# Optimization experiments

Hardware: AMD Instinct MI355X
Metric: run time of the kernel (lower is better)

## Reference

```python
import jax, jax.numpy as jnp
import numpy as np

N_HEADS = 16

def _rotate_half(t):
    # t: [B, H, T, hs]; split last dim in half, return cat(-x2, x1)
    hs = t.shape[-1]
    x1, x2 = t[..., : hs // 2], t[..., hs // 2 :]
    return jnp.concatenate((-x2, x1), axis=-1)

def _rope_pos(T, hs, dtype):
    inv_freq = 1.0 / (10000.0 ** (jnp.arange(0, hs, 2, dtype=jnp.float32) / hs))
    freqs = jnp.arange(T, dtype=jnp.float32)[:, None] * inv_freq[None, :]  # [T, hs/2]
    pos = jnp.concatenate((freqs, freqs), axis=-1)  # [T, hs]
    return pos

def setup_inputs() -> dict:
    key = jax.random.key(0)
    ks = jax.random.split(key, 5)
    d = 2048
    x = jax.random.normal(ks[0], (2, 2048, d), dtype=jnp.float32)
    W_attn = jax.random.normal(ks[1], (d, 3 * d), dtype=jnp.float32) * (1.0 / np.sqrt(d))
    b_attn = jax.random.normal(ks[2], (3 * d,), dtype=jnp.float32) * 0.02
    W_proj = jax.random.normal(ks[3], (d, d), dtype=jnp.float32) * (1.0 / np.sqrt(d))
    b_proj = jax.random.normal(ks[4], (d,), dtype=jnp.float32) * 0.02
    return {"x": x, "W_attn": W_attn, "b_attn": b_attn, "W_proj": W_proj, "b_proj": b_proj}

def reference(x, W_attn, b_attn, W_proj, b_proj):
    B, T, C = x.shape
    nh = N_HEADS
    hs = C // nh
    qkv = x @ W_attn + b_attn  # [B, T, 3C]
    q, k, v = jnp.split(qkv, 3, axis=-1)
    # [B, T, C] -> [B, nh, T, hs]
    def to_heads(t):
        return t.reshape(B, T, nh, hs).transpose(0, 2, 1, 3)
    q, k, v = to_heads(q), to_heads(k), to_heads(v)
    # RoPE
    pos = _rope_pos(T, hs, x.dtype)  # [T, hs]
    cos, sin = jnp.cos(pos).astype(x.dtype), jnp.sin(pos).astype(x.dtype)
    q = q * cos + _rotate_half(q) * sin
    k = k * cos + _rotate_half(k) * sin
    # causal SDPA
    scale = 1.0 / np.sqrt(hs)
    scores = jnp.einsum('bhqd,bhkd->bhqk', q, k) * scale  # [B, nh, T, T]
    causal = jnp.tril(jnp.ones((T, T), dtype=bool))
    scores = jnp.where(causal, scores, jnp.finfo(scores.dtype).min)
    att = jax.nn.softmax(scores, axis=-1)
    out = jnp.einsum('bhqk,bhkd->bhqd', att, v)  # [B, nh, T, hs]
    y = out.transpose(0, 2, 1, 3).reshape(B, T, C)
    return y @ W_proj + b_proj
```

## Files before the change

kernel.cpp:

```cpp
#include <hip/hip_runtime.h>
#include <stdint.h>

typedef unsigned short u16;
typedef __attribute__((ext_vector_type(8))) short short8;
typedef __attribute__((ext_vector_type(4))) float f32x4;
typedef __attribute__((ext_vector_type(4))) unsigned short u16x4;

#define DEV __device__ __forceinline__

DEV u16 f2bf(float f) {
  union { float f; unsigned u; } v; v.f = f;
  unsigned r = v.u + 0x7fffu + ((v.u >> 16) & 1u);
  return (u16)(r >> 16);
}
DEV float bf2f(u16 b) {
  union { unsigned u; float f; } v; v.u = ((unsigned)b) << 16;
  return v.f;
}
DEV void gload_lds16(const void* g, void* l) {
  __builtin_amdgcn_global_load_lds((const __attribute__((address_space(1))) void*)g,
                                   (__attribute__((address_space(3))) void*)l,
                                   16, 0, 0);
}
DEV void block_barrier() {
  asm volatile("" ::: "memory");
  __builtin_amdgcn_s_barrier();
  asm volatile("" ::: "memory");
}

__global__ void k_conv(const float* __restrict__ in, u16* __restrict__ out, int n4) {
  int i = blockIdx.x * blockDim.x + threadIdx.x;
  if (i >= n4) return;
  const f32x4 v = *(const f32x4*)(in + (size_t)i * 4);
  u16x4 o;
  o[0] = f2bf(v[0]); o[1] = f2bf(v[1]); o[2] = f2bf(v[2]); o[3] = f2bf(v[3]);
  *(u16x4*)(out + (size_t)i * 4) = o;
}

__global__ void k_tconv(const float* __restrict__ in, u16* __restrict__ out, int R, int C) {
  __shared__ float tile[32][33];
  int c0 = blockIdx.x * 32, r0 = blockIdx.y * 32;
  int tx = threadIdx.x, ty = threadIdx.y;
#pragma unroll
  for (int j = 0; j < 32; j += 8)
    tile[ty + j][tx] = in[(size_t)(r0 + ty + j) * C + (c0 + tx)];
  __syncthreads();
#pragma unroll
  for (int j = 0; j < 32; j += 8)
    out[(size_t)(c0 + ty + j) * R + (r0 + tx)] = f2bf(tile[tx][ty + j]);
}

__global__ __launch_bounds__(512, 2) void k_gemmqkv(const u16* __restrict__ A,
                                                    const u16* __restrict__ Bt,
                                                    const float* __restrict__ bias,
                                                    u16* __restrict__ qh,
                                                    u16* __restrict__ kh,
                                                    u16* __restrict__ vt) {
  const int Kld = 2048, nt = 32;
  __shared__ __align__(16) short smem[4][256 * 64];
  const int tid = threadIdx.x;
  const int wid = tid >> 6, lane = tid & 63;
  const int gx = gridDim.x;
  const int nwg = gx * gridDim.y;
  const int orig = blockIdx.y * gx + blockIdx.x;
  const int lg = (orig & 7) * (nwg >> 3) + (orig >> 3);
  const int bm = (lg % gx) * 256, bn = (lg / gx) * 256;
  const int wr = wid >> 2, wc = wid & 3;
  const int r = lane & 15, kq = lane >> 4, r7 = lane & 7;

  int aoff[4], boff[4], lbase[4];
#pragma unroll
  for (int j = 0; j < 4; ++j) {
    int c = j * 512 + wid * 64 + lane;
    int row = c >> 3, ch = c & 7;
    aoff[j] = (bm + row) * Kld + (ch ^ (row & 7)) * 8;
    boff[j] = (bn + row) * Kld + (ch ^ (row & 7)) * 8;
    lbase[j] = (j * 512 + wid * 64) * 16;
  }

#define STG_A(k0, buf, j) gload_lds16(A + aoff[j] + (k0), (char*)&smem[(buf)][0] + lbase[j])
#define STG_B(k0, buf, j) gload_lds16(Bt + boff[j] + (k0), (char*)&smem[2 + (buf)][0] + lbase[j])
#define RD_A(AF, MH, KK)                                                        \
  _Pragma("unroll")                                                             \
  for (int m2 = 0; m2 < 4; ++m2)                                                \
    AF[m2] = *(const short8*)&As[(wr * 128 + (MH) * 64 + m2 * 16 + r) * 64      \
                                 + (((KK) * 4 + kq) ^ r7) * 8];
#define RD_B(KK)                                                                \
  _Pragma("unroll")                                                             \
  for (int nf = 0; nf < 4; ++nf)                                                \
    bfr[KK][nf] = *(const short8*)&Bs[(wc * 64 + nf * 16 + r) * 64              \
                                      + (((KK) * 4 + kq) ^ r7) * 8];
#define PH_MFMA(AF, MH, KK)                                                     \
  __builtin_amdgcn_s_setprio(1);                                                \
  _Pragma("unroll")                                                             \
  for (int m2 = 0; m2 < 4; ++m2)                                                \
    _Pragma("unroll")                                                           \
    for (int nf = 0; nf < 4; ++nf)                                              \
      acc[(MH) * 4 + m2][nf] = __builtin_amdgcn_mfma_f32_16x16x32_bf16(         \
          AF[m2], bfr[KK][nf], acc[(MH) * 4 + m2][nf], 0, 0, 0);                \
  __builtin_amdgcn_s_setprio(0);

  f32x4 acc[8][4];
  const f32x4 zero = {0.f, 0.f, 0.f, 0.f};
#pragma unroll
  for (int i = 0; i < 8; ++i)
#pragma unroll
    for (int j = 0; j < 4; ++j) acc[i][j] = zero;

#pragma unroll
  for (int j = 0; j < 4; ++j) STG_A(0, 0, j);
#pragma unroll
  for (int j = 0; j < 4; ++j) STG_B(0, 0, j);
#pragma unroll
  for (int j = 0; j < 4; ++j) STG_B(64, 1, j);
  asm volatile("s_waitcnt vmcnt(4)" ::: "memory");
  block_barrier();

#pragma unroll 1
  for (int t = 0; t < nt; ++t) {
    const int cur = t & 1, nxt = cur ^ 1;
    const short* As = &smem[cur][0];
    const short* Bs = &smem[2 + cur][0];
    const int kA = (t + 1) * 64, kB = (t + 2) * 64;
    const bool sA = (t + 1 < nt), sB = (t + 2 < nt);
    short8 bfr[2][4];
    short8 af[4];

    RD_B(0)
    RD_A(af, 0, 0)
    if (sA) { STG_A(kA, nxt, 0); STG_A(kA, nxt, 1); }
    block_barrier();
    PH_MFMA(af, 0, 0)
    block_barrier();

    RD_B(1)
    RD_A(af, 0, 1)
    if (sA) { STG_A(kA, nxt, 2); STG_A(kA, nxt, 3); }
    block_barrier();
    PH_MFMA(af, 0, 1)
    block_barrier();

    RD_A(af, 1, 0)
    if (sB) { STG_B(kB, cur, 0); STG_B(kB, cur, 1); }
    block_barrier();
    PH_MFMA(af, 1, 0)
    block_barrier();

    RD_A(af, 1, 1)
    if (sB) { STG_B(kB, cur, 2); STG_B(kB, cur, 3); }
    block_barrier();
    PH_MFMA(af, 1, 1)
    if (t + 1 < nt) {
      if (sB) asm volatile("s_waitcnt vmcnt(4)" ::: "memory");
      else    asm volatile("s_waitcnt vmcnt(0)" ::: "memory");
    }
    block_barrier();
  }
#undef STG_A
#undef STG_B
#undef RD_A
#undef RD_B
#undef PH_MFMA

  const int by = lg / gx;
  const int part = by >> 3;
  const int b_ = bm >> 11;
  const int tb = bm & 2047;
  const int hbase = (bn & 2047) >> 7;
  u16* ob = (u16*)&smem[0][0];

#pragma unroll
  for (int nf = 0; nf < 4; ++nf) {
    int nl = wc * 64 + nf * 16 + r;
    float bv = bias[bn + nl];
#pragma unroll
    for (int mf = 0; mf < 8; ++mf) {
      int mlb = wr * 128 + mf * 16 + kq * 4;
#pragma unroll
      for (int i = 0; i < 4; ++i) {
        int ml = mlb + i;
        int cl = (part == 2)
          ? (nl ^ (((ml >> 2) & 3) << 4) ^ (((ml >> 4) & 7) << 1))
          : (nl ^ (((ml >> 2) & 3) << 4));
        ob[ml * 256 + cl] = f2bf(acc[mf][nf][i] + bv);
      }
    }
  }
  block_barrier();

  if (part == 2) {
#pragma unroll 1
    for (int iter = 0; iter < 32; ++iter) {
      int dl = iter * 8 + wid;
      int hh = hbase + (dl >> 7), d = dl & 127;
      int tl4 = lane * 4;
      int cl = dl ^ ((lane & 3) << 4) ^ (((lane >> 2) & 7) << 1);
      u16x4 o;
#pragma unroll
      for (int j = 0; j < 4; ++j) o[j] = ob[(tl4 + j) * 256 + cl];
      *(u16x4*)(vt + ((size_t)(b_ * 16 + hh) * 128 + d) * 2048 + tb + tl4) = o;
    }
  } else {
    u16* dst = part ? kh : qh;
    const float qscale = part ? 1.0f : 0.12751744766834352f;
    const int nl2 = lane * 4;
    const int hh = hbase + (nl2 >> 7);
    const int d0 = nl2 & 127;
    const int hi = (nl2 >> 6) & 1;
    float inv0 = exp2f((float)(nl2 & 63) * -0.20762050593045077f);
    const float k1 = 0.8659643233600653f;
    float invj[4];
    invj[0] = inv0; invj[1] = inv0 * k1; invj[2] = invj[1] * k1; invj[3] = invj[2] * k1;
#pragma unroll 1
    for (int iter = 0; iter < 32; ++iter) {
      int tl = iter * 8 + wid;
      float tg = (float)(tb + tl);
      int xr = ((tl >> 2) & 3) << 4;
      int base = tl * 256 + (nl2 ^ xr);
      int pbase = tl * 256 + ((nl2 ^ 64) ^ xr);
      u16x4 o;
#pragma unroll
      for (int j = 0; j < 4; ++j) {
        float vo = bf2f(ob[base + j]);
        float vp = bf2f(ob[pbase + j]);
        float sn, cs;
        sincosf(tg * invj[j], &sn, &cs);
        float vr = hi ? (vo * cs + vp * sn) : (vo * cs - vp * sn);
        o[j] = f2bf(vr * qscale);
      }
      *(u16x4*)(dst + ((size_t)(b_ * 16 + hh) * 2048 + (tb + tl)) * 128 + d0) = o;
    }
  }
}

template <bool OUT_BF16, bool SPLITK>
__global__ __launch_bounds__(512, 2) void k_gemm3(const u16* __restrict__ A,
                                                  const u16* __restrict__ Bt,
                                                  const float* __restrict__ bias,
                                                  void* __restrict__ Cv,
                                                  int M, int N, int Kld, int nkt) {
  __shared__ __align__(16) short lA[2][256 * 64];
  __shared__ __align__(16) short lB[2][256 * 64];
  const int tid = threadIdx.x;
  const int wid = tid >> 6, lane = tid & 63;
  const int gx = gridDim.x;
  const int nwg = gx * gridDim.y;
  const int orig = blockIdx.y * gx + blockIdx.x;
  const int lg = (orig & 7) * (nwg >> 3) + (orig >> 3);
  const int bm = (lg % gx) * 256, bn = (lg / gx) * 256;
  const int wr = wid >> 2, wc = wid & 3;
  const int r = lane & 15, kq = lane >> 4, r7 = lane & 7;
  const int kz = SPLITK ? blockIdx.z * (nkt << 6) : 0;

  int aoff[4], boff[4], lbase[4];
#pragma unroll
  for (int j = 0; j < 4; ++j) {
    int c = j * 512 + wid * 64 + lane;
    int row = c >> 3, ch = c & 7;
    aoff[j] = (bm + row) * Kld + kz + (ch ^ (row & 7)) * 8;
    boff[j] = (bn + row) * Kld + kz + (ch ^ (row & 7)) * 8;
    lbase[j] = (j * 512 + wid * 64) * 16;
  }

#define STG_A(k0, buf, j) gload_lds16(A + aoff[j] + (k0), (char*)&lA[(buf)][0] + lbase[j])
#define STG_B(k0, buf, j) gload_lds16(Bt + boff[j] + (k0), (char*)&lB[(buf)][0] + lbase[j])
#define RD_A(AF, MH, KK)                                                        \
  _Pragma("unroll")                                                             \
  for (int m2 = 0; m2 < 4; ++m2)                                                \
    AF[m2] = *(const short8*)&As[(wr * 128 + (MH) * 64 + m2 * 16 + r) * 64      \
                                 + (((KK) * 4 + kq) ^ r7) * 8];
#define RD_B(KK)                                                                \
  _Pragma("unroll")                                                             \
  for (int nf = 0; nf < 4; ++nf)                                                \
    bfr[KK][nf] = *(const short8*)&Bs[(wc * 64 + nf * 16 + r) * 64              \
                                      + (((KK) * 4 + kq) ^ r7) * 8];
#define PH_MFMA(AF, MH, KK)                                                     \
  __builtin_amdgcn_s_setprio(1);                                                \
  _Pragma("unroll")                                                             \
  for (int m2 = 0; m2 < 4; ++m2)                                                \
    _Pragma("unroll")                                                           \
    for (int nf = 0; nf < 4; ++nf)                                              \
      acc[(MH) * 4 + m2][nf] = __builtin_amdgcn_mfma_f32_16x16x32_bf16(         \
          AF[m2], bfr[KK][nf], acc[(MH) * 4 + m2][nf], 0, 0, 0);                \
  __builtin_amdgcn_s_setprio(0);

  f32x4 acc[8][4];
  const f32x4 zero = {0.f, 0.f, 0.f, 0.f};
#pragma unroll
  for (int i = 0; i < 8; ++i)
#pragma unroll
    for (int j = 0; j < 4; ++j) acc[i][j] = zero;

  const int nt = nkt;

#pragma unroll
  for (int j = 0; j < 4; ++j) STG_A(0, 0, j);
#pragma unroll
  for (int j = 0; j < 4; ++j) STG_B(0, 0, j);
  if (nt > 1) {
#pragma unroll
    for (int j = 0; j < 4; ++j) STG_B(64, 1, j);
    asm volatile("s_waitcnt vmcnt(4)" ::: "memory");
  } else {
    asm volatile("s_waitcnt vmcnt(0)" ::: "memory");
  }
  block_barrier();

#pragma unroll 1
  for (int t = 0; t < nt; ++t) {
    const int cur = t & 1, nxt = cur ^ 1;
    const short* As = &lA[cur][0];
    const short* Bs = &lB[cur][0];
    const int kA = (t + 1) * 64, kB = (t + 2) * 64;
    const bool sA = (t + 1 < nt), sB = (t + 2 < nt);
    short8 bfr[2][4];
    short8 af[4];

    RD_B(0)
    RD_A(af, 0, 0)
    if (sA) { STG_A(kA, nxt, 0); STG_A(kA, nxt, 1); }
    block_barrier();
    PH_MFMA(af, 0, 0)
    block_barrier();

    RD_B(1)
    RD_A(af, 0, 1)
    if (sA) { STG_A(kA, nxt, 2); STG_A(kA, nxt, 3); }
    block_barrier();
    PH_MFMA(af, 0, 1)
    block_barrier();

    RD_A(af, 1, 0)
    if (sB) { STG_B(kB, cur, 0); STG_B(kB, cur, 1); }
    block_barrier();
    PH_MFMA(af, 1, 0)
    block_barrier();

    RD_A(af, 1, 1)
    if (sB) { STG_B(kB, cur, 2); STG_B(kB, cur, 3); }
    block_barrier();
    PH_MFMA(af, 1, 1)
    if (t + 1 < nt) {
      if (sB) asm volatile("s_waitcnt vmcnt(4)" ::: "memory");
      else    asm volatile("s_waitcnt vmcnt(0)" ::: "memory");
    }
    block_barrier();
  }
#undef STG_A
#undef STG_B
#undef RD_A
#undef RD_B
#undef PH_MFMA

#pragma unroll
  for (int mf = 0; mf < 8; ++mf)
#pragma unroll
    for (int nf = 0; nf < 4; ++nf) {
      int n = bn + wc * 64 + nf * 16 + r;
      float bv = SPLITK ? 0.f : bias[n];
#pragma unroll
      for (int i = 0; i < 4; ++i) {
        int m = bm + wr * 128 + mf * 16 + kq * 4 + i;
        float val = acc[mf][nf][i] + bv;
        if (SPLITK)
          ((float*)Cv)[(size_t)blockIdx.z * M * N + (size_t)m * N + n] = val;
        else if (OUT_BF16)
          ((u16*)Cv)[(size_t)m * N + n] = f2bf(val);
        else
          ((float*)Cv)[(size_t)m * N + n] = val;
      }
    }
}

__global__ void k_fadd(const float* __restrict__ p, const float* __restrict__ bias,
                       float* __restrict__ y, int n4) {
  const int half4 = 2097152;
  for (int i = blockIdx.x * blockDim.x + threadIdx.x; i < n4; i += gridDim.x * blockDim.x) {
    f32x4 a = *(const f32x4*)(p + (size_t)i * 4);
    f32x4 b = *(const f32x4*)(p + (size_t)(i + half4) * 4);
    f32x4 bv = *(const f32x4*)(bias + ((i & 511) << 2));
    f32x4 o = a + b + bv;
    *(f32x4*)(y + (size_t)i * 4) = o;
  }
}

__global__ __launch_bounds__(256) void k_attn(const u16* __restrict__ qh,
                                              const u16* __restrict__ kh,
                                              const u16* __restrict__ vt,
                                              u16* __restrict__ out) {
  __shared__ __align__(16) short lK[2][64 * 128];
  __shared__ __align__(16) short lV[2][128 * 64];
  __shared__ __align__(16) short lP[64 * 64];
  const int tid = threadIdx.x, wid = tid >> 6, lane = tid & 63;
  const int p = blockIdx.x, h = blockIdx.y, b = blockIdx.z;
  const size_t bh = (size_t)b * 16 + h;
  const u16* qb = qh + bh * 2048 * 128;
  const u16* kb = kh + bh * 2048 * 128;
  const u16* vb = vt + bh * 128 * 2048;
  const int r = lane & 15, kq = lane >> 4;
  const int r7 = r & 7;
  const int wrow = wid * 16;

  int koff[4], voff[4];
#pragma unroll
  for (int i = 0; i < 4; ++i) {
    int ci = (wid * 4 + i) * 64 + lane;
    int krow = ci >> 4, kch = ci & 15;
    koff[i] = krow * 128 + ((kch ^ (krow & 7)) * 8);
    int vrow = ci >> 3, vch = ci & 7;
    voff[i] = vrow * 2048 + ((vch ^ (vrow & 7)) * 8);
  }

#pragma unroll 1
  for (int seg = 0; seg < 2; ++seg) {
    const int j = seg ? 31 - p : p;
    const int q0 = j * 64;
    const int nkt = j + 1;

    short8 qa[4];
#pragma unroll
    for (int kk = 0; kk < 4; ++kk)
      qa[kk] = *(const short8*)(qb + (size_t)(q0 + wrow + r) * 128 + kk * 32 + kq * 8);

    f32x4 O[8];
    const f32x4 zero = {0.f, 0.f, 0.f, 0.f};
#pragma unroll
    for (int nf = 0; nf < 8; ++nf) O[nf] = zero;
    float lp[4] = {0.f, 0.f, 0.f, 0.f};

#pragma unroll
    for (int i = 0; i < 4; ++i) {
      gload_lds16(kb + koff[i], (char*)&lK[0][0] + (wid * 4 + i) * 1024);
      gload_lds16(vb + voff[i], (char*)&lV[0][0] + (wid * 4 + i) * 1024);
    }

#pragma unroll 1
    for (int kt = 0; kt < nkt; ++kt) {
      const int cur = kt & 1;
      if (kt + 1 < nkt) {
        const size_t kbase = (size_t)(kt + 1) * 8192, vbase = (size_t)(kt + 1) * 64;
#pragma unroll
        for (int i = 0; i < 4; ++i) {
          gload_lds16(kb + kbase + koff[i], (char*)&lK[cur ^ 1][0] + (wid * 4 + i) * 1024);
          gload_lds16(vb + vbase + voff[i], (char*)&lV[cur ^ 1][0] + (wid * 4 + i) * 1024);
        }
        asm volatile("s_waitcnt vmcnt(8)" ::: "memory");
      } else {
        asm volatile("s_waitcnt vmcnt(0)" ::: "memory");
      }
      block_barrier();

      f32x4 S[4];
#pragma unroll
      for (int nf = 0; nf < 4; ++nf) S[nf] = zero;
#pragma unroll
      for (int kk = 0; kk < 4; ++kk) {
        short8 kf[4];
#pragma unroll
        for (int nf = 0; nf < 4; ++nf)
          kf[nf] = *(const short8*)&lK[cur][(nf * 16 + r) * 128 + ((kk * 4 + kq) ^ r7) * 8];
#pragma unroll
        for (int nf = 0; nf < 4; ++nf)
          S[nf] = __builtin_amdgcn_mfma_f32_16x16x32_bf16(qa[kk], kf[nf], S[nf], 0, 0, 0);
      }

      const bool diag = (kt == nkt - 1);
#pragma unroll
      for (int nf = 0; nf < 4; ++nf)
#pragma unroll
        for (int i = 0; i < 4; ++i) {
          float pv = exp2f(S[nf][i]);
          if (diag) {
            int kg = kt * 64 + nf * 16 + r;
            int qg = q0 + wrow + kq * 4 + i;
            pv = (kg > qg) ? 0.f : pv;
          }
          lp[i] += pv;
          int row = wrow + kq * 4 + i;
          int cl = (nf * 2 + (r >> 3)) ^ ((kq * 4 + i) & 7);
          lP[row * 64 + cl * 8 + r7] = (short)f2bf(pv);
        }

#pragma unroll
      for (int kk = 0; kk < 2; ++kk) {
        short8 pa = *(const short8*)&lP[(wrow + r) * 64 + ((kk * 4 + kq) ^ r7) * 8];
#pragma unroll
        for (int nf = 0; nf < 8; ++nf) {
          short8 vf = *(const short8*)&lV[cur][(nf * 16 + r) * 64 + ((kk * 4 + kq) ^ r7) * 8];
          O[nf] = __builtin_amdgcn_mfma_f32_16x16x32_bf16(pa, vf, O[nf], 0, 0, 0);
        }
      }
      asm volatile("s_waitcnt lgkmcnt(0)" ::: "memory");
      block_barrier();
    }

    float inv[4];
#pragma unroll
    for (int i = 0; i < 4; ++i) {
      float v = lp[i];
      v += __shfl_xor(v, 1);
      v += __shfl_xor(v, 2);
      v += __shfl_xor(v, 4);
      v += __shfl_xor(v, 8);
      inv[i] = 1.f / v;
    }
#pragma unroll
    for (int nf = 0; nf < 8; ++nf)
#pragma unroll
      for (int i = 0; i < 4; ++i) {
        int qg = q0 + wrow + kq * 4 + i;
        out[(size_t)(b * 2048 + qg) * 2048 + h * 128 + nf * 16 + r] = f2bf(O[nf][i] * inv[i]);
      }
  }
}

extern "C" void kernel_launch(void* const* d_in, const int* in_sizes, int n_in,
                              void* d_out, int out_size, void* d_ws, size_t ws_size,
                              hipStream_t stream) {
  const float* x      = (const float*)d_in[0];
  const float* W_attn = (const float*)d_in[1];
  const float* b_attn = (const float*)d_in[2];
  const float* W_proj = (const float*)d_in[3];
  const float* b_proj = (const float*)d_in[4];
  float* y = (float*)d_out;

  u16* xb     = (u16*)d_ws;
  u16* wqkvT  = xb     + (size_t)4096 * 2048;
  u16* wprojT = wqkvT  + (size_t)6144 * 2048;
  u16* qkv    = wprojT + (size_t)2048 * 2048;
  u16* qh     = qkv    + (size_t)4096 * 6144;
  u16* kh     = qh     + (size_t)4096 * 2048;
  u16* vt     = kh     + (size_t)4096 * 2048;
  u16* attout = vt     + (size_t)4096 * 2048;
  if (ws_size < (size_t)83886080 * 2) return;

  float* pproj = (float*)qkv;

  k_conv<<<8192, 256, 0, stream>>>(x, xb, 2097152);
  k_tconv<<<dim3(192, 64), dim3(32, 8), 0, stream>>>(W_attn, wqkvT, 2048, 6144);
  k_tconv<<<dim3(64, 64), dim3(32, 8), 0, stream>>>(W_proj, wprojT, 2048, 2048);
  k_gemmqkv<<<dim3(16, 24), 512, 0, stream>>>(xb, wqkvT, b_attn, qh, kh, vt);
  k_attn<<<dim3(16, 16, 2), 256, 0, stream>>>(qh, kh, vt, attout);
  k_gemm3<false, true><<<dim3(16, 8, 2), 512, 0, stream>>>(attout, wprojT, b_proj, pproj, 4096, 2048, 2048, 16);
  k_fadd<<<2048, 256, 0, stream>>>(pproj, b_proj, y, 2097152);
}
```

Measured before the change: 319.8 us.

## Precompute RoPE sin/cos table and widen attention blocks to 128 query rows

Adds a small kernel that precomputes cos/sin tables for RoPE so the QKV GEMM epilogue loads them instead of calling sincosf per element. The attention kernel now uses 512 threads (8 waves) covering 128 query rows per block, halving the grid and sharing each K/V tile load across twice as many query rows. The diagonal masking now spans two key tiles. This trades more LDS and a larger block for less redundant K/V traffic and less transcendental work, and it reduces the number of blocks available for load balancing.

```diff
diff --git a/kernel.cpp b/kernel.cpp
--- a/kernel.cpp
+++ b/kernel.cpp
@@ -50,12 +50,22 @@
     out[(size_t)(c0 + ty + j) * R + (r0 + tx)] = f2bf(tile[tx][ty + j]);
 }
 
+__global__ void k_rtab(float* __restrict__ ct, float* __restrict__ st) {
+  int id = blockIdx.x * 256 + threadIdx.x;
+  int t = id >> 6, dd = id & 63;
+  float inv = exp2f((float)dd * -0.20762050593045077f);
+  float s, c;
+  sincosf((float)t * inv, &s, &c);
+  ct[id] = c; st[id] = s;
+}
+
 __global__ __launch_bounds__(512, 2) void k_gemmqkv(const u16* __restrict__ A,
                                                     const u16* __restrict__ Bt,
                                                     const float* __restrict__ bias,
                                                     u16* __restrict__ qh,
                                                     u16* __restrict__ kh,
-                                                    u16* __restrict__ vt) {
+                                                    u16* __restrict__ vt,
+                                                    const float* __restrict__ rtab) {
   const int Kld = 2048, nt = 32;
   __shared__ __align__(16) short smem[4][256 * 64];
   const int tid = threadIdx.x;
@@ -207,14 +217,15 @@
     const int hh = hbase + (nl2 >> 7);
     const int d0 = nl2 & 127;
     const int hi = (nl2 >> 6) & 1;
-    float inv0 = exp2f((float)(nl2 & 63) * -0.20762050593045077f);
-    const float k1 = 0.8659643233600653f;
-    float invj[4];
-    invj[0] = inv0; invj[1] = inv0 * k1; invj[2] = invj[1] * k1; invj[3] = invj[2] * k1;
-#pragma unroll 1
+    const int dd4 = nl2 & 63;
+    const float* ct = rtab;
+    const float* st = rtab + 131072;
+#pragma unroll 2
     for (int iter = 0; iter < 32; ++iter) {
       int tl = iter * 8 + wid;
-      float tg = (float)(tb + tl);
+      int tg = tb + tl;
+      f32x4 c4 = *(const f32x4*)(ct + tg * 64 + dd4);
+      f32x4 s4 = *(const f32x4*)(st + tg * 64 + dd4);
       int xr = ((tl >> 2) & 3) << 4;
       int base = tl * 256 + (nl2 ^ xr);
       int pbase = tl * 256 + ((nl2 ^ 64) ^ xr);
@@ -223,12 +234,10 @@
       for (int j = 0; j < 4; ++j) {
         float vo = bf2f(ob[base + j]);
         float vp = bf2f(ob[pbase + j]);
-        float sn, cs;
-        sincosf(tg * invj[j], &sn, &cs);
-        float vr = hi ? (vo * cs + vp * sn) : (vo * cs - vp * sn);
+        float vr = hi ? (vo * c4[j] + vp * s4[j]) : (vo * c4[j] - vp * s4[j]);
         o[j] = f2bf(vr * qscale);
       }
-      *(u16x4*)(dst + ((size_t)(b_ * 16 + hh) * 2048 + (tb + tl)) * 128 + d0) = o;
+      *(u16x4*)(dst + ((size_t)(b_ * 16 + hh) * 2048 + tg) * 128 + d0) = o;
     }
   }
 }
@@ -384,13 +393,13 @@
   }
 }
 
-__global__ __launch_bounds__(256) void k_attn(const u16* __restrict__ qh,
+__global__ __launch_bounds__(512) void k_attn(const u16* __restrict__ qh,
                                               const u16* __restrict__ kh,
                                               const u16* __restrict__ vt,
                                               u16* __restrict__ out) {
   __shared__ __align__(16) short lK[2][64 * 128];
   __shared__ __align__(16) short lV[2][128 * 64];
-  __shared__ __align__(16) short lP[64 * 64];
+  __shared__ __align__(16) short lP[128 * 64];
   const int tid = threadIdx.x, wid = tid >> 6, lane = tid & 63;
   const int p = blockIdx.x, h = blockIdx.y, b = blockIdx.z;
   const size_t bh = (size_t)b * 16 + h;
@@ -401,21 +410,22 @@
   const int r7 = r & 7;
   const int wrow = wid * 16;
 
-  int koff[4], voff[4];
-#pragma unroll
-  for (int i = 0; i < 4; ++i) {
-    int ci = (wid * 4 + i) * 64 + lane;
-    int krow = ci >> 4, kch = ci & 15;
+  int koff[2], voff[2], lbase[2];
+#pragma unroll
+  for (int i = 0; i < 2; ++i) {
+    int c = i * 512 + wid * 64 + lane;
+    int krow = c >> 4, kch = c & 15;
     koff[i] = krow * 128 + ((kch ^ (krow & 7)) * 8);
-    int vrow = ci >> 3, vch = ci & 7;
+    int vrow = c >> 3, vch = c & 7;
     voff[i] = vrow * 2048 + ((vch ^ (vrow & 7)) * 8);
+    lbase[i] = (i * 512 + wid * 64) * 16;
   }
 
 #pragma unroll 1
   for (int seg = 0; seg < 2; ++seg) {
-    const int j = seg ? 31 - p : p;
-    const int q0 = j * 64;
-    const int nkt = j + 1;
+    const int J = seg ? 15 - p : p;
+    const int q0 = J * 128;
+    const int nkt = 2 * J + 2;
 
     short8 qa[4];
 #pragma unroll
@@ -429,9 +439,9 @@
     float lp[4] = {0.f, 0.f, 0.f, 0.f};
 
 #pragma unroll
-    for (int i = 0; i < 4; ++i) {
-      gload_lds16(kb + koff[i], (char*)&lK[0][0] + (wid * 4 + i) * 1024);
-      gload_lds16(vb + voff[i], (char*)&lV[0][0] + (wid * 4 + i) * 1024);
+    for (int i = 0; i < 2; ++i) {
+      gload_lds16(kb + koff[i], (char*)&lK[0][0] + lbase[i]);
+      gload_lds16(vb + voff[i], (char*)&lV[0][0] + lbase[i]);
     }
 
 #pragma unroll 1
@@ -440,11 +450,11 @@
       if (kt + 1 < nkt) {
         const size_t kbase = (size_t)(kt + 1) * 8192, vbase = (size_t)(kt + 1) * 64;
 #pragma unroll
-        for (int i = 0; i < 4; ++i) {
-          gload_lds16(kb + kbase + koff[i], (char*)&lK[cur ^ 1][0] + (wid * 4 + i) * 1024);
-          gload_lds16(vb + vbase + voff[i], (char*)&lV[cur ^ 1][0] + (wid * 4 + i) * 1024);
+        for (int i = 0; i < 2; ++i) {
+          gload_lds16(kb + kbase + koff[i], (char*)&lK[cur ^ 1][0] + lbase[i]);
+          gload_lds16(vb + vbase + voff[i], (char*)&lV[cur ^ 1][0] + lbase[i]);
         }
-        asm volatile("s_waitcnt vmcnt(8)" ::: "memory");
+        asm volatile("s_waitcnt vmcnt(4)" ::: "memory");
       } else {
         asm volatile("s_waitcnt vmcnt(0)" ::: "memory");
       }
@@ -464,7 +474,7 @@
           S[nf] = __builtin_amdgcn_mfma_f32_16x16x32_bf16(qa[kk], kf[nf], S[nf], 0, 0, 0);
       }
 
-      const bool diag = (kt == nkt - 1);
+      const bool diag = (kt >= nkt - 2);
 #pragma unroll
       for (int nf = 0; nf < 4; ++nf)
 #pragma unroll
@@ -534,13 +544,15 @@
   u16* attout = vt     + (size_t)4096 * 2048;
   if (ws_size < (size_t)83886080 * 2) return;
 
+  float* rtab  = (float*)qkv;
   float* pproj = (float*)qkv;
 
   k_conv<<<8192, 256, 0, stream>>>(x, xb, 2097152);
   k_tconv<<<dim3(192, 64), dim3(32, 8), 0, stream>>>(W_attn, wqkvT, 2048, 6144);
   k_tconv<<<dim3(64, 64), dim3(32, 8), 0, stream>>>(W_proj, wprojT, 2048, 2048);
-  k_gemmqkv<<<dim3(16, 24), 512, 0, stream>>>(xb, wqkvT, b_attn, qh, kh, vt);
-  k_attn<<<dim3(16, 16, 2), 256, 0, stream>>>(qh, kh, vt, attout);
+  k_rtab<<<512, 256, 0, stream>>>(rtab, rtab + 131072);
+  k_gemmqkv<<<dim3(16, 24), 512, 0, stream>>>(xb, wqkvT, b_attn, qh, kh, vt, rtab);
+  k_attn<<<dim3(8, 16, 2), 512, 0, stream>>>(qh, kh, vt, attout);
   k_gemm3<false, true><<<dim3(16, 8, 2), 512, 0, stream>>>(attout, wprojT, b_proj, pproj, 4096, 2048, 2048, 16);
   k_fadd<<<2048, 256, 0, stream>>>(pproj, b_proj, y, 2097152);
 }
```

Measured after the change: 297.1 us. 7.1% less time.
